# Kernel optimization log

Hardware: AMD Instinct MI355X
Metric: run time of the kernel (lower is better)

## Reference

```python
import jax, jax.numpy as jnp
import numpy as np
from jax import lax

DIM = 128
HEADS = 8
GROUPS = 8
DIM_HEAD = 64
DOWN = 4
OFF_SCALE = 4.0
KSIZE = 6
B, N, M = 2, 1024, 1024


def ln(x, g, b, eps=1e-5):
    m = x.mean(-1, keepdims=True)
    v = ((x - m) ** 2).mean(-1, keepdims=True)
    return (x - m) / jnp.sqrt(v + eps) * g + b


def grid_sample_1d(feats, grid):
    # feats: (Bg, C, Mk), grid: (Bg, Nd) normalized coords in [-1, 1]
    # bilinear, padding_mode='zeros', align_corners=False (torch semantics)
    Bg, C, Mk = feats.shape
    x = ((grid + 1.0) * Mk - 1.0) / 2.0
    x0 = jnp.floor(x)
    w1 = x - x0

    def gather(xi):
        valid = ((xi >= 0) & (xi <= Mk - 1)).astype(feats.dtype)
        idx = jnp.clip(xi, 0, Mk - 1).astype(jnp.int32)
        vals = jnp.take_along_axis(
            feats, jnp.broadcast_to(idx[:, None, :], (Bg, C, idx.shape[-1])), axis=2)
        return vals * valid[:, None, :]

    return gather(x0) * (1.0 - w1)[:, None, :] + gather(x0 + 1.0) * w1[:, None, :]


def deform_cross_attn(xq, xkv, qw, kw, vw, ow, ob, o1w, o1b, o2w,
                      c1w, c1b, c2w, c2b, c3w, c3b):
    # xq, xkv: (B, C, N) channel-first token streams
    Bb, C, Nq = xq.shape
    cg = C // GROUPS  # 16 channels per offset group
    q = jnp.einsum('bgcn,goc->bgon', xq.reshape(Bb, GROUPS, cg, Nq), qw)  # (B,g,64,N)
    gq = q.reshape(Bb * GROUPS, DIM_HEAD, Nq)
    pad = (KSIZE - DOWN) // 2
    off = lax.conv_general_dilated(gq, o1w[:, None, :], (DOWN,), [(pad, pad)],
                                   feature_group_count=DIM_HEAD,
                                   dimension_numbers=('NCH', 'OIH', 'NCH')) + o1b[None, :, None]
    off = jax.nn.gelu(off, approximate=False)
    off = jnp.tanh(jnp.einsum('bcn,c->bn', off, o2w)) * OFF_SCALE  # (B*g, Nd)
    Nd = off.shape[-1]
    vgrid = jnp.arange(Nd, dtype=off.dtype)[None] + off
    vgs = 2.0 * vgrid / max(Nd - 1, 1) - 1.0  # normalized sample positions
    xkv_g = xkv.reshape(Bb, GROUPS, cg, xkv.shape[-1]).reshape(Bb * GROUPS, cg, xkv.shape[-1])
    kv = grid_sample_1d(xkv_g, vgs).reshape(Bb, GROUPS, cg, Nd)
    k = jnp.einsum('bgcn,goc->bgon', kv, kw)
    v = jnp.einsum('bgcn,goc->bgon', kv, vw)
    sim = jnp.einsum('bhdi,bhdj->bhij', q * (DIM_HEAD ** -0.5), k)  # heads == groups
    seq = 2.0 * jnp.arange(Nq, dtype=vgs.dtype) / max(Nq - 1, 1) - 1.0
    rel = seq[None, :, None] - vgs[:, None, :]  # (B*g, N, Nd)
    bias = jnp.sign(rel) * jnp.log1p(jnp.abs(rel))
    h = jax.nn.relu(bias[..., None] * c1w[0] + c1b)  # CPB MLP, hidden=dim//4=32
    h = jax.nn.relu(h @ c2w + c2b)
    h = (h @ c3w + c3b)[..., 0]
    sim = sim + h.reshape(Bb, GROUPS, Nq, Nd)  # heads // offset_groups == 1
    attn = jax.nn.softmax(sim, axis=-1)
    out = jnp.einsum('bhij,bhdj->bhdi', attn, v).reshape(Bb, GROUPS * DIM_HEAD, Nq)
    out = jnp.einsum('bcn,oc->bon', out, ow) + ob[:, None]
    return out, attn


def mha(q_in, kv_in, w_in, b_in, w_out, b_out):
    # seq-first torch nn.MultiheadAttention, eval mode (no dropout)
    E = DIM; h = HEADS; dh = E // h
    q = q_in @ w_in[:E].T + b_in[:E]
    k = kv_in @ w_in[E:2 * E].T + b_in[E:2 * E]
    v = kv_in @ w_in[2 * E:].T + b_in[2 * E:]
    Lq, Bb, _ = q.shape
    Lk = k.shape[0]
    qh = q.reshape(Lq, Bb, h, dh).transpose(1, 2, 0, 3)
    kh = k.reshape(Lk, Bb, h, dh).transpose(1, 2, 0, 3)
    vh = v.reshape(Lk, Bb, h, dh).transpose(1, 2, 0, 3)
    attn = jax.nn.softmax(jnp.einsum('bhid,bhjd->bhij', qh, kh) * (dh ** -0.5), axis=-1)
    out = jnp.einsum('bhij,bhjd->bhid', attn, vh).transpose(2, 0, 1, 3).reshape(Lq, Bb, E)
    return out @ w_out.T + b_out


def transfusion(x1, x2, ng, nb, inw, inb, ow, ob, pw, pb):
    x = x1 + mha(ln(x1, ng, nb), ln(x2, ng, nb), inw, inb, ow, ob)
    x = ln(x.transpose(1, 0, 2), ng, nb)  # (B, N, E)
    return jnp.tanh(x.mean(1) @ pw.T + pb)[:, None, :]  # (B, 1, E)


def setup_inputs():
    key = jax.random.key(0)
    ks = iter(jax.random.split(key, 40))
    rn = lambda shape, s=0.05: jax.random.normal(next(ks), shape, dtype=jnp.float32) * s
    return {
        'x1_0': rn((B, N, DIM), 1.0),
        'x1_1': rn((B, N, DIM), 1.0),
        'x2': rn((B, M, DIM), 1.0),
        'norm_g': jnp.ones((DIM,), jnp.float32),
        'norm_b': jnp.zeros((DIM,), jnp.float32),
        'd_qw': rn((2, GROUPS, DIM_HEAD, DIM // GROUPS)),
        'd_kw': rn((2, GROUPS, DIM_HEAD, DIM // GROUPS)),
        'd_vw': rn((2, GROUPS, DIM_HEAD, DIM // GROUPS)),
        'd_ow': rn((2, DIM, GROUPS * DIM_HEAD)),
        'd_ob': jnp.zeros((2, DIM), jnp.float32),
        'd_off1w': rn((2, DIM_HEAD, KSIZE)),
        'd_off1b': jnp.zeros((2, DIM_HEAD), jnp.float32),
        'd_off2w': rn((2, DIM_HEAD)),
        'd_cpb_w1': rn((2, 1, 32)),
        'd_cpb_b1': jnp.zeros((2, 32), jnp.float32),
        'd_cpb_w2': rn((2, 32, 32)),
        'd_cpb_b2': jnp.zeros((2, 32), jnp.float32),
        'd_cpb_w3': rn((2, 32, 1)),
        'd_cpb_b3': jnp.zeros((2, 1), jnp.float32),
        'fus_w': rn((DIM, 2 * DIM)),
        'fus_b': jnp.zeros((DIM,), jnp.float32),
        'tf_ng': jnp.ones((2, DIM), jnp.float32),
        'tf_nb': jnp.zeros((2, DIM), jnp.float32),
        'tf_inw': rn((2, 3 * DIM, DIM)),
        'tf_inb': jnp.zeros((2, 3 * DIM), jnp.float32),
        'tf_ow': rn((2, DIM, DIM)),
        'tf_ob': jnp.zeros((2, DIM), jnp.float32),
        'tf_pw': rn((2, DIM, DIM)),
        'tf_pb': jnp.zeros((2, DIM), jnp.float32),
        'attn_dim': 128,
    }


def reference(x1_0, x1_1, x2, norm_g, norm_b, d_qw, d_kw, d_vw, d_ow, d_ob,
              d_off1w, d_off1b, d_off2w, d_cpb_w1, d_cpb_b1, d_cpb_w2, d_cpb_b2,
              d_cpb_w3, d_cpb_b3, fus_w, fus_b, tf_ng, tf_nb, tf_inw, tf_inb,
              tf_ow, tf_ob, tf_pw, tf_pb, attn_dim):
    nkv = ln(x2, norm_g, norm_b).transpose(0, 2, 1)
    xo1, a1 = deform_cross_attn(ln(x1_0, norm_g, norm_b).transpose(0, 2, 1), nkv,
                                d_qw[0], d_kw[0], d_vw[0], d_ow[0], d_ob[0],
                                d_off1w[0], d_off1b[0], d_off2w[0],
                                d_cpb_w1[0], d_cpb_b1[0], d_cpb_w2[0], d_cpb_b2[0],
                                d_cpb_w3[0], d_cpb_b3[0])
    xo2, a2 = deform_cross_attn(ln(x1_1, norm_g, norm_b).transpose(0, 2, 1), nkv,
                                d_qw[1], d_kw[1], d_vw[1], d_ow[1], d_ob[1],
                                d_off1w[1], d_off1b[1], d_off2w[1],
                                d_cpb_w1[1], d_cpb_b1[1], d_cpb_w2[1], d_cpb_b2[1],
                                d_cpb_w3[1], d_cpb_b3[1])
    xout1 = x1_0 + xo1.transpose(0, 2, 1)
    xout2 = x1_1 + xo2.transpose(0, 2, 1)
    x = jnp.concatenate([xout1, xout2], axis=-1) @ fus_w.T + fus_b
    query = ln(x, norm_g, norm_b).transpose(1, 0, 2)
    kv1 = ln(x1_0[:, :1, :], norm_g, norm_b).transpose(1, 0, 2)
    kv2 = ln(x1_1[:, :1, :], norm_g, norm_b).transpose(1, 0, 2)
    f1 = transfusion(query, kv1, tf_ng[0], tf_nb[0], tf_inw[0], tf_inb[0],
                     tf_ow[0], tf_ob[0], tf_pw[0], tf_pb[0])
    f2 = transfusion(query, kv2, tf_ng[1], tf_nb[1], tf_inw[1], tf_inb[1],
                     tf_ow[1], tf_ob[1], tf_pw[1], tf_pb[1])
    return (f1, f2, a1, a2)
```

## Files before the change

### kernel.cpp

```cpp
#include <hip/hip_runtime.h>
#include <hip/hip_bf16.h>


namespace {

constexpr int kN  = 1024;
constexpr int kC  = 128;
constexpr int kG  = 8;
constexpr int kDH = 64;
constexpr int kND = 256;

constexpr int   kNT    = 16384;
constexpr float kRLO   = -2.0625f;
constexpr float kRSPAN = 4.125f;

constexpr size_t W_LNKV = 0;
constexpr size_t W_LNQ1 = 262144;
constexpr size_t W_LNQ2 = 524288;
constexpr size_t W_Q    = 786432;
constexpr size_t W_K    = 1835008;
constexpr size_t W_VT   = 2097152;
constexpr size_t W_VGS  = 2359296;
constexpr size_t W_AO   = 2367488;
constexpr size_t W_FUS  = 4988928;
constexpr size_t W_TAB  = 5251072;
constexpr size_t W_MOUT = 5283844;
constexpr size_t W_PART = 5284356;
constexpr size_t W_OWB  = 5317124;
constexpr size_t W_FWB  = 5382660;

}

typedef __attribute__((ext_vector_type(8))) short short8;
typedef __attribute__((ext_vector_type(4))) float floatx4;

__device__ __forceinline__ float wave_sum(float v) {
#pragma unroll
  for (int o = 32; o > 0; o >>= 1) v += __shfl_xor(v, o, 64);
  return v;
}
__device__ __forceinline__ float cpb_bias(const float* __restrict__ tabs,
                                          float seq, float vg) {
  float rel = seq - vg;
  float ft = (rel - kRLO) * ((float)kNT / kRSPAN);
  ft = fminf(fmaxf(ft, 0.f), 16383.999f);
  int ix = (int)ft;
  float fw = ft - (float)ix;
  return tabs[ix] * (1.f - fw) + tabs[ix + 1] * fw;
}

__global__ void k_prep(const float* __restrict__ ow, const float* __restrict__ fw,
                       __hip_bfloat16* __restrict__ owb, __hip_bfloat16* __restrict__ fwb,
                       const float* __restrict__ x1_0, const float* __restrict__ x1_1,
                       const float* __restrict__ x2, float* __restrict__ lnq1,
                       float* __restrict__ lnq2, float* __restrict__ lnkv,
                       const float* __restrict__ ng, const float* __restrict__ nb,
                       const float* __restrict__ cw1, const float* __restrict__ cb1,
                       const float* __restrict__ cw2, const float* __restrict__ cb2,
                       const float* __restrict__ cw3, const float* __restrict__ cb3,
                       float* __restrict__ tab,
                       const float* __restrict__ tfng, const float* __restrict__ tfnb,
                       const float* __restrict__ inw, const float* __restrict__ inb,
                       const float* __restrict__ tow, const float* __restrict__ tob,
                       float* __restrict__ mout) {
  int bx = blockIdx.x;
  int t = threadIdx.x;
  if (bx < 640) {
    int id = bx * 256 + t;
    if (id < 131072) owb[id] = __float2bfloat16(ow[id]);
    else fwb[id - 131072] = __float2bfloat16(fw[id - 131072]);
  } else if (bx < 2176) {
    int w = t >> 6, lane = t & 63;
    int gr = (bx - 640) * 4 + w;
    int sel = gr >> 11, row = gr & 2047;
    const float* in = (sel == 0) ? x1_0 : (sel == 1) ? x1_1 : x2;
    float* out = (sel == 0) ? lnq1 : (sel == 1) ? lnq2 : lnkv;
    const float* xr = in + (size_t)row * kC;
    float xa = xr[lane], xb = xr[lane + 64];
    float m = wave_sum(xa + xb) * (1.f / kC);
    float da = xa - m, db = xb - m;
    float v = wave_sum(da * da + db * db) * (1.f / kC);
    float r = rsqrtf(v + 1e-5f);
    float* orow = out + (size_t)row * kC;
    orow[lane]      = da * r * ng[lane] + nb[lane];
    orow[lane + 64] = db * r * ng[lane + 64] + nb[lane + 64];
  } else if (bx < 2306) {
    int rel = bx - 2176;
    int idx = rel / 65, bb = rel - idx * 65;
    int tt = bb * 256 + t;
    if (tt <= kNT) {
      float rel_ = kRLO + (kRSPAN / (float)kNT) * (float)tt;
      float u = (rel_ >= 0.f ? 1.f : -1.f) * log1pf(fabsf(rel_));
      const float* W1 = cw1 + idx * 32; const float* B1 = cb1 + idx * 32;
      const float* W2 = cw2 + idx * 1024; const float* B2 = cb2 + idx * 32;
      const float* W3 = cw3 + idx * 32; const float* B3 = cb3 + idx;
      float h1[32];
#pragma unroll
      for (int m = 0; m < 32; ++m) h1[m] = fmaxf(0.f, u * W1[m] + B1[m]);
      float o = B3[0];
      for (int m = 0; m < 32; ++m) {
        float a = B2[m];
#pragma unroll
        for (int k = 0; k < 32; ++k) a += h1[k] * W2[k * 32 + m];
        o += fmaxf(a, 0.f) * W3[m];
      }
      tab[(size_t)idx * (kNT + 1) + tt] = o;
    }
  } else {
    int rel = bx - 2306;
    int i = rel >> 1, b = rel & 1;
    bool act = t < 128;
    __shared__ float red[2];
    __shared__ float s1[128];
    __shared__ float s2[128];
    const float* xs = (i ? x1_1 : x1_0) + (size_t)b * kN * kC;
    float x = act ? xs[t] : 0.f;
    float s = wave_sum(x);
    if (act && (t & 63) == 0) red[t >> 6] = s;
    __syncthreads();
    float m1 = (red[0] + red[1]) * (1.f / kC);
    __syncthreads();
    float d1 = x - m1;
    float ss = wave_sum(act ? d1 * d1 : 0.f);
    if (act && (t & 63) == 0) red[t >> 6] = ss;
    __syncthreads();
    float v1 = (red[0] + red[1]) * (1.f / kC);
    __syncthreads();
    float t0 = act ? d1 * rsqrtf(v1 + 1e-5f) * ng[t] + nb[t] : 0.f;
    s = wave_sum(t0);
    if (act && (t & 63) == 0) red[t >> 6] = s;
    __syncthreads();
    float m2 = (red[0] + red[1]) * (1.f / kC);
    __syncthreads();
    float d2 = t0 - m2;
    ss = wave_sum(act ? d2 * d2 : 0.f);
    if (act && (t & 63) == 0) red[t >> 6] = ss;
    __syncthreads();
    float v2 = (red[0] + red[1]) * (1.f / kC);
    if (act) s1[t] = d2 * rsqrtf(v2 + 1e-5f) * tfng[i * kC + t] + tfnb[i * kC + t];
    __syncthreads();
    if (act) {
      float a0 = 0.f;
      const float* wr = inw + (size_t)i * 384 * kC + (size_t)(256 + t) * kC;
      for (int c = 0; c < 128; ++c) a0 += s1[c] * wr[c];
      s2[t] = inb[i * 384 + 256 + t] + a0;
    }
    __syncthreads();
    if (act) {
      float a0 = 0.f;
      const float* wr2 = tow + (size_t)i * kC * kC + (size_t)t * kC;
      for (int c = 0; c < 128; ++c) a0 += s2[c] * wr2[c];
      mout[rel * kC + t] = tob[i * kC + t] + a0;
    }
  }
}

__global__ void k_qoff(const float* __restrict__ lnq1, const float* __restrict__ lnq2,
                       const float* __restrict__ qw, const float* __restrict__ o1w,
                       const float* __restrict__ o1b, const float* __restrict__ o2w,
                       __hip_bfloat16* __restrict__ qout, float* __restrict__ vgs) {
  int bx = blockIdx.x;
  if (bx < 512) {
    int bg = bx >> 4, r0 = (bx & 15) * 64;
    int str = bg >> 4, b = (bg >> 3) & 1, g = bg & 7;
    int rl = threadIdx.x & 63, dq = threadIdx.x >> 6;
    const float* lnq = str ? lnq2 : lnq1;
    const float* xr = lnq + ((size_t)(b * kN + r0 + rl)) * kC + g * 16;
    float4 x0 = *(const float4*)(xr + 0);
    float4 x1 = *(const float4*)(xr + 4);
    float4 x2 = *(const float4*)(xr + 8);
    float4 x3 = *(const float4*)(xr + 12);
    const float* wqb = qw + (size_t)str * 8192 + (size_t)g * 1024;
    __hip_bfloat16* qrow = qout + ((size_t)bg * 1024 + r0 + rl) * 64 + dq * 16;
#pragma unroll 4
    for (int dd = 0; dd < 16; ++dd) {
      int d = dq * 16 + dd;
      const float* wq = wqb + d * 16;
      float4 w0 = *(const float4*)(wq + 0);
      float4 w1 = *(const float4*)(wq + 4);
      float4 w2 = *(const float4*)(wq + 8);
      float4 w3 = *(const float4*)(wq + 12);
      float q = x0.x * w0.x + x0.y * w0.y + x0.z * w0.z + x0.w * w0.w
              + x1.x * w1.x + x1.y * w1.y + x1.z * w1.z + x1.w * w1.w
              + x2.x * w2.x + x2.y * w2.y + x2.z * w2.z + x2.w * w2.w
              + x3.x * w3.x + x3.y * w3.y + x3.z * w3.z + x3.w * w3.w;
      qrow[dd] = __float2bfloat16(q);
    }
  } else {
    int bxo = bx - 512;
    int w = threadIdx.x >> 6, lane = threadIdx.x & 63;
    int bg = bxo >> 6, j = ((bxo & 63) << 2) + w;
    int str = bg >> 4, b = (bg >> 3) & 1, g = bg & 7;
    const float* lnq = str ? lnq2 : lnq1;
    __shared__ float xr[4][96];
    int base = j * 4 - 1;
#pragma unroll
    for (int rep = 0; rep < 2; ++rep) {
      int idx = lane + rep * 64;
      if (idx < 96) {
        int r = idx >> 4, c = idx & 15, n = base + r;
        xr[w][idx] = (n >= 0 && n < kN)
                         ? lnq[((size_t)(b * kN + n)) * kC + g * 16 + c] : 0.f;
      }
    }
    const float* wq = qw + (size_t)str * 8192 + (size_t)(g * kDH + lane) * 16;
    float acc = o1b[str * 64 + lane];
#pragma unroll
    for (int k2 = 0; k2 < 6; ++k2) {
      float qv = 0.f;
#pragma unroll
      for (int c = 0; c < 16; ++c) qv += xr[w][k2 * 16 + c] * wq[c];
      acc += qv * o1w[str * 384 + lane * 6 + k2];
    }
    float ge = 0.5f * acc * (1.f + erff(acc * 0.70710678118654752440f));
    float s = wave_sum(ge * o2w[str * 64 + lane]);
    if (lane == 0)
      vgs[bg * kND + j] = 2.f * ((float)j + tanhf(s) * 4.0f) / 255.f - 1.f;
  }
}

__global__ void k_sample_kv(const float* __restrict__ lnkv, const float* __restrict__ vgs,
                            const float* __restrict__ kw, const float* __restrict__ vw,
                            __hip_bfloat16* __restrict__ kout,
                            __hip_bfloat16* __restrict__ vtout) {
  int w = threadIdx.x >> 6, lane = threadIdx.x & 63;
  int bg = blockIdx.x >> 6, j = ((blockIdx.x & 63) << 2) + w;
  int str = bg >> 4, b = (bg >> 3) & 1, g = bg & 7;
  __shared__ float sc[4][16];
  if (lane < 16) {
    float gr = vgs[bg * kND + j];
    float x = ((gr + 1.f) * 1024.f - 1.f) * 0.5f;
    float x0f = floorf(x);
    float w1 = x - x0f;
    int x0 = (int)x0f, x1 = x0 + 1;
    const float* src = lnkv + (size_t)b * kN * kC + g * 16 + lane;
    float v0 = (x0 >= 0 && x0 < 1024) ? src[(size_t)x0 * kC] : 0.f;
    float v1 = (x1 >= 0 && x1 < 1024) ? src[(size_t)x1 * kC] : 0.f;
    sc[w][lane] = v0 * (1.f - w1) + v1 * w1;
  }
  const float* kwr = kw + (size_t)str * 8192 + (size_t)(g * kDH + lane) * 16;
  const float* vwr = vw + (size_t)str * 8192 + (size_t)(g * kDH + lane) * 16;
  float ka = 0.f, va = 0.f;
#pragma unroll
  for (int c = 0; c < 16; ++c) { ka += sc[w][c] * kwr[c]; va += sc[w][c] * vwr[c]; }
  kout[((size_t)bg * 256 + j) * 64 + lane] = __float2bfloat16(ka);
  vtout[((size_t)bg * 64 + lane) * 256 + j] = __float2bfloat16(va);
}

__global__ void __launch_bounds__(256, 2)
k_attn(const __hip_bfloat16* __restrict__ q_g, const __hip_bfloat16* __restrict__ k_g,
       const __hip_bfloat16* __restrict__ vt_g, const float* __restrict__ vgs,
       const float* __restrict__ tab, float* __restrict__ aout,
       __hip_bfloat16* __restrict__ attout) {
  int bg = blockIdx.x >> 4, tile = blockIdx.x & 15;
  int str = bg >> 4;
  int i0 = tile * 64;
  int t = threadIdx.x;
  int w = t >> 6, l = t & 63;
  int lr = l & 15, lg = l >> 4;

  __shared__ __align__(16) __hip_bfloat16 Qs[64 * 72];
  __shared__ __align__(16) __hip_bfloat16 Ss[64 * 72];
  __shared__ __align__(16) __hip_bfloat16 Ps[64 * 272];

  const float* tabs = tab + str * (kNT + 1);

  {
    int r = t >> 2, c0 = (t & 3) * 16;
    const __hip_bfloat16* src = q_g + ((size_t)bg * 1024 + i0 + r) * 64 + c0;
    *(float4*)&Qs[r * 72 + c0]     = *(const float4*)src;
    *(float4*)&Qs[r * 72 + c0 + 8] = *(const float4*)(src + 8);
  }
  short8 a0 = *(const short8*)&Qs[(w * 16 + lr) * 72 + lg * 8];
  short8 a1 = *(const short8*)&Qs[(w * 16 + lr) * 72 + 32 + lg * 8];

  floatx4 acc[16];
#pragma unroll
  for (int f = 0; f < 16; ++f) acc[f] = {0.f, 0.f, 0.f, 0.f};

#pragma unroll
  for (int jc = 0; jc < 4; ++jc) {
    __syncthreads();
    {
      int r = t >> 2, c0 = (t & 3) * 16;
      const __hip_bfloat16* src = k_g + ((size_t)bg * 256 + jc * 64 + r) * 64 + c0;
      *(float4*)&Ss[r * 72 + c0]     = *(const float4*)src;
      *(float4*)&Ss[r * 72 + c0 + 8] = *(const float4*)(src + 8);
    }
    __syncthreads();
#pragma unroll
    for (int ct = 0; ct < 4; ++ct) {
      short8 b0 = *(const short8*)&Ss[(ct * 16 + lr) * 72 + lg * 8];
      short8 b1 = *(const short8*)&Ss[(ct * 16 + lr) * 72 + 32 + lg * 8];
      acc[jc * 4 + ct] =
          __builtin_amdgcn_mfma_f32_16x16x32_bf16(a0, b0, acc[jc * 4 + ct], 0, 0, 0);
      acc[jc * 4 + ct] =
          __builtin_amdgcn_mfma_f32_16x16x32_bf16(a1, b1, acc[jc * 4 + ct], 0, 0, 0);
    }
  }

  float vgl[16];
#pragma unroll
  for (int f = 0; f < 16; ++f) vgl[f] = vgs[bg * 256 + f * 16 + lr];
  float* aoutb = aout + (size_t)str * 4194304 + (size_t)(bg & 15) * 262144;
#pragma unroll
  for (int reg = 0; reg < 4; ++reg) {
    int row = w * 16 + lg * 4 + reg;
    int i = i0 + row;
    float seq = 2.f * (float)i / 1023.f - 1.f;
    float sv[16];
#pragma unroll
    for (int f = 0; f < 16; ++f)
      sv[f] = acc[f][reg] * 0.125f + cpb_bias(tabs, seq, vgl[f]);
    float m = sv[0];
#pragma unroll
    for (int f = 1; f < 16; ++f) m = fmaxf(m, sv[f]);
    m = fmaxf(m, __shfl_xor(m, 1, 64));
    m = fmaxf(m, __shfl_xor(m, 2, 64));
    m = fmaxf(m, __shfl_xor(m, 4, 64));
    m = fmaxf(m, __shfl_xor(m, 8, 64));
    float ev[16], sum = 0.f;
#pragma unroll
    for (int f = 0; f < 16; ++f) { ev[f] = expf(sv[f] - m); sum += ev[f]; }
    sum += __shfl_xor(sum, 1, 64);
    sum += __shfl_xor(sum, 2, 64);
    sum += __shfl_xor(sum, 4, 64);
    sum += __shfl_xor(sum, 8, 64);
    float inv = 1.f / sum;
    float* arow = aoutb + (size_t)i * 256;
#pragma unroll
    for (int f = 0; f < 16; ++f) {
      float p = ev[f] * inv;
      arow[f * 16 + lr] = p;
      Ps[row * 272 + f * 16 + lr] = __float2bfloat16(p);
    }
  }

  floatx4 oacc[4];
#pragma unroll
  for (int dt = 0; dt < 4; ++dt) oacc[dt] = {0.f, 0.f, 0.f, 0.f};
#pragma unroll
  for (int jc = 0; jc < 4; ++jc) {
    __syncthreads();
    {
      int r = t >> 2, c0 = (t & 3) * 16;
      const __hip_bfloat16* src = vt_g + ((size_t)bg * 64 + r) * 256 + jc * 64 + c0;
      *(float4*)&Ss[r * 72 + c0]     = *(const float4*)src;
      *(float4*)&Ss[r * 72 + c0 + 8] = *(const float4*)(src + 8);
    }
    __syncthreads();
    short8 pa0 = *(const short8*)&Ps[(w * 16 + lr) * 272 + jc * 64 + lg * 8];
    short8 pa1 = *(const short8*)&Ps[(w * 16 + lr) * 272 + jc * 64 + 32 + lg * 8];
#pragma unroll
    for (int dt = 0; dt < 4; ++dt) {
      short8 b0 = *(const short8*)&Ss[(dt * 16 + lr) * 72 + lg * 8];
      short8 b1 = *(const short8*)&Ss[(dt * 16 + lr) * 72 + 32 + lg * 8];
      oacc[dt] = __builtin_amdgcn_mfma_f32_16x16x32_bf16(pa0, b0, oacc[dt], 0, 0, 0);
      oacc[dt] = __builtin_amdgcn_mfma_f32_16x16x32_bf16(pa1, b1, oacc[dt], 0, 0, 0);
    }
  }
  {
    int b = (bg >> 3) & 1, g = bg & 7;
    __hip_bfloat16* ab = attout + ((size_t)(str * 2 + b) * 1024) * 512 + (size_t)g * 64;
#pragma unroll
    for (int dt = 0; dt < 4; ++dt)
#pragma unroll
      for (int reg = 0; reg < 4; ++reg) {
        int row = w * 16 + lg * 4 + reg;
        ab[(size_t)(i0 + row) * 512 + dt * 16 + lr] = __float2bfloat16(oacc[dt][reg]);
      }
  }
}

__global__ void __launch_bounds__(256, 2)
k_oproj_fuse(const __hip_bfloat16* __restrict__ aog, const __hip_bfloat16* __restrict__ owb,
             const float* __restrict__ ob,
             const float* __restrict__ x1_0, const float* __restrict__ x1_1,
             const __hip_bfloat16* __restrict__ fwb, const float* __restrict__ fb,
             float* __restrict__ fused) {
  int tok0 = blockIdx.x * 16;
  int t = threadIdx.x;
  int w = t >> 6, l = t & 63;
  int lr = l & 15, lg = l >> 4;
  int nt0 = w * 2;

  __shared__ __align__(16) __hip_bfloat16 xos[16 * 280];

  for (int s = 0; s < 2; ++s) {
    const __hip_bfloat16* arow = aog + ((size_t)(s * 2048 + tok0 + lr)) * 512 + lg * 8;
    const __hip_bfloat16* wb0 = owb + (size_t)s * 65536 + (size_t)((nt0 + 0) * 16 + lr) * 512 + lg * 8;
    const __hip_bfloat16* wb1 = owb + (size_t)s * 65536 + (size_t)((nt0 + 1) * 16 + lr) * 512 + lg * 8;
    floatx4 acc0 = {0.f, 0.f, 0.f, 0.f}, acc1 = {0.f, 0.f, 0.f, 0.f};
#pragma unroll
    for (int ks = 0; ks < 16; ++ks) {
      short8 a  = *(const short8*)(arow + ks * 32);
      short8 b0 = *(const short8*)(wb0 + ks * 32);
      short8 b1 = *(const short8*)(wb1 + ks * 32);
      acc0 = __builtin_amdgcn_mfma_f32_16x16x32_bf16(a, b0, acc0, 0, 0, 0);
      acc1 = __builtin_amdgcn_mfma_f32_16x16x32_bf16(a, b1, acc1, 0, 0, 0);
    }
    const float* x1 = s ? x1_1 : x1_0;
    float bias0 = ob[s * 128 + nt0 * 16 + lr];
    float bias1 = ob[s * 128 + (nt0 + 1) * 16 + lr];
#pragma unroll
    for (int reg = 0; reg < 4; ++reg) {
      int row = lg * 4 + reg;
      size_t xi = (size_t)(tok0 + row) * 128;
      xos[row * 280 + s * 128 + nt0 * 16 + lr] =
          __float2bfloat16(acc0[reg] + x1[xi + nt0 * 16 + lr] + bias0);
      xos[row * 280 + s * 128 + (nt0 + 1) * 16 + lr] =
          __float2bfloat16(acc1[reg] + x1[xi + (nt0 + 1) * 16 + lr] + bias1);
    }
  }
  __syncthreads();

  floatx4 f0 = {0.f, 0.f, 0.f, 0.f}, f1 = {0.f, 0.f, 0.f, 0.f};
  const __hip_bfloat16* fb0 = fwb + (size_t)((nt0 + 0) * 16 + lr) * 256 + lg * 8;
  const __hip_bfloat16* fb1 = fwb + (size_t)((nt0 + 1) * 16 + lr) * 256 + lg * 8;
#pragma unroll
  for (int ks = 0; ks < 8; ++ks) {
    short8 a  = *(const short8*)&xos[lr * 280 + ks * 32 + lg * 8];
    short8 b0 = *(const short8*)(fb0 + ks * 32);
    short8 b1 = *(const short8*)(fb1 + ks * 32);
    f0 = __builtin_amdgcn_mfma_f32_16x16x32_bf16(a, b0, f0, 0, 0, 0);
    f1 = __builtin_amdgcn_mfma_f32_16x16x32_bf16(a, b1, f1, 0, 0, 0);
  }
  float fbias0 = fb[nt0 * 16 + lr], fbias1 = fb[(nt0 + 1) * 16 + lr];
#pragma unroll
  for (int reg = 0; reg < 4; ++reg) {
    int row = lg * 4 + reg;
    fused[(size_t)(tok0 + row) * 128 + nt0 * 16 + lr]       = f0[reg] + fbias0;
    fused[(size_t)(tok0 + row) * 128 + (nt0 + 1) * 16 + lr] = f1[reg] + fbias1;
  }
}

__global__ void k_meanz(const float* __restrict__ fused, const float* __restrict__ ng,
                        const float* __restrict__ nb, const float* __restrict__ tfng,
                        const float* __restrict__ tfnb, const float* __restrict__ mout,
                        float* __restrict__ partial) {
  int chunk = blockIdx.x, b = blockIdx.y, i = blockIdx.z;
  int w = threadIdx.x >> 6, lane = threadIdx.x & 63;
  int c = lane, c2 = lane + 64;
  float moa = mout[(i * 2 + b) * kC + c], mob = mout[(i * 2 + b) * kC + c2];
  float g1a = ng[c], b1a = nb[c], g1b = ng[c2], b1b = nb[c2];
  float g2a = tfng[i * kC + c], b2a = tfnb[i * kC + c];
  float g2b = tfng[i * kC + c2], b2b = tfnb[i * kC + c2];
  float acca = 0.f, accb = 0.f;
#pragma unroll
  for (int it = 0; it < 4; ++it) {
    int tok = chunk * 16 + it * 4 + w;
    const float* xr = fused + ((size_t)(b * kN + tok)) * kC;
    float xa = xr[c], xb = xr[c2];
    float m1 = wave_sum(xa + xb) * (1.f / kC);
    float da = xa - m1, db = xb - m1;
    float v1 = wave_sum(da * da + db * db) * (1.f / kC);
    float r1 = rsqrtf(v1 + 1e-5f);
    float za = da * r1 * g1a + b1a + moa;
    float zb = db * r1 * g1b + b1b + mob;
    float m2 = wave_sum(za + zb) * (1.f / kC);
    float ea = za - m2, eb = zb - m2;
    float v2 = wave_sum(ea * ea + eb * eb) * (1.f / kC);
    float r2 = rsqrtf(v2 + 1e-5f);
    acca += ea * r2 * g2a + b2a;
    accb += eb * r2 * g2b + b2b;
  }
  __shared__ float red[4][128];
  red[w][c] = acca; red[w][c2] = accb;
  __syncthreads();
  if (w == 0) {
    float pa = red[0][c] + red[1][c] + red[2][c] + red[3][c];
    float pb = red[0][c2] + red[1][c2] + red[2][c2] + red[3][c2];
    float* pr = partial + ((size_t)(i * 2 + b) * 64 + chunk) * kC;
    pr[c] = pa; pr[c2] = pb;
  }
}

__global__ void k_final(const float* __restrict__ partial, const float* __restrict__ pw,
                        const float* __restrict__ pb, float* __restrict__ out) {
  int ib = blockIdx.x;
  int i = ib >> 1, t = threadIdx.x;
  int c = t & 127, half = t >> 7;
  float a = 0.f;
  for (int ch = half * 32; ch < half * 32 + 32; ++ch)
    a += partial[((size_t)ib * 64 + ch) * kC + c];
  __shared__ float s[256];
  s[half * 128 + c] = a;
  __syncthreads();
  if (t < 128) s[t] = (s[t] + s[128 + t]) * (1.f / (float)kN);
  __syncthreads();
  if (t < 128) {
    float a0 = 0.f;
    const float* wr = pw + (size_t)i * kC * kC + (size_t)t * kC;
    for (int cc = 0; cc < 128; ++cc) a0 += s[cc] * wr[cc];
    out[ib * 128 + t] = tanhf(pb[i * kC + t] + a0);
  }
}

extern "C" void kernel_launch(void* const* d_in, const int* in_sizes, int n_in,
                              void* d_out, int out_size, void* d_ws, size_t ws_size,
                              hipStream_t stream) {
  const float* x1_0   = (const float*)d_in[0];
  const float* x1_1   = (const float*)d_in[1];
  const float* x2     = (const float*)d_in[2];
  const float* norm_g = (const float*)d_in[3];
  const float* norm_b = (const float*)d_in[4];
  const float* d_qw   = (const float*)d_in[5];
  const float* d_kw   = (const float*)d_in[6];
  const float* d_vw   = (const float*)d_in[7];
  const float* d_ow   = (const float*)d_in[8];
  const float* d_ob   = (const float*)d_in[9];
  const float* d_o1w  = (const float*)d_in[10];
  const float* d_o1b  = (const float*)d_in[11];
  const float* d_o2w  = (const float*)d_in[12];
  const float* c_w1   = (const float*)d_in[13];
  const float* c_b1   = (const float*)d_in[14];
  const float* c_w2   = (const float*)d_in[15];
  const float* c_b2   = (const float*)d_in[16];
  const float* c_w3   = (const float*)d_in[17];
  const float* c_b3   = (const float*)d_in[18];
  const float* fus_w  = (const float*)d_in[19];
  const float* fus_b  = (const float*)d_in[20];
  const float* tf_ng  = (const float*)d_in[21];
  const float* tf_nb  = (const float*)d_in[22];
  const float* tf_inw = (const float*)d_in[23];
  const float* tf_inb = (const float*)d_in[24];
  const float* tf_ow  = (const float*)d_in[25];
  const float* tf_ob  = (const float*)d_in[26];
  const float* tf_pw  = (const float*)d_in[27];
  const float* tf_pb  = (const float*)d_in[28];

  float* ws = (float*)d_ws;
  float* out = (float*)d_out;
  float* lnkv = ws + W_LNKV;
  float* lnq1 = ws + W_LNQ1; float* lnq2 = ws + W_LNQ2;
  __hip_bfloat16* qb  = (__hip_bfloat16*)(ws + W_Q);
  __hip_bfloat16* kb  = (__hip_bfloat16*)(ws + W_K);
  __hip_bfloat16* vtb = (__hip_bfloat16*)(ws + W_VT);
  float* vgsw = ws + W_VGS;
  __hip_bfloat16* aob = (__hip_bfloat16*)(ws + W_AO);
  float* fused = ws + W_FUS; float* tab = ws + W_TAB;
  float* moutp = ws + W_MOUT; float* partp = ws + W_PART;
  __hip_bfloat16* owb = (__hip_bfloat16*)(ws + W_OWB);
  __hip_bfloat16* fwb = (__hip_bfloat16*)(ws + W_FWB);

  float* aoutb = out + 512;

  k_prep<<<2310, 256, 0, stream>>>(d_ow, fus_w, owb, fwb,
                                   x1_0, x1_1, x2, lnq1, lnq2, lnkv, norm_g, norm_b,
                                   c_w1, c_b1, c_w2, c_b2, c_w3, c_b3, tab,
                                   tf_ng, tf_nb, tf_inw, tf_inb, tf_ow, tf_ob, moutp);
  k_qoff<<<2560, 256, 0, stream>>>(lnq1, lnq2, d_qw, d_o1w, d_o1b, d_o2w, qb, vgsw);
  k_sample_kv<<<2048, 256, 0, stream>>>(lnkv, vgsw, d_kw, d_vw, kb, vtb);
  k_attn<<<512, 256, 0, stream>>>(qb, kb, vtb, vgsw, tab, aoutb, aob);
  k_oproj_fuse<<<128, 256, 0, stream>>>(aob, owb, d_ob, x1_0, x1_1, fwb, fus_b, fused);
  k_meanz<<<dim3(64, 2, 2), 256, 0, stream>>>(fused, norm_g, norm_b, tf_ng, tf_nb,
                                              moutp, partp);
  k_final<<<4, 256, 0, stream>>>(partp, tf_pw, tf_pb, out);

  (void)in_sizes; (void)n_in; (void)out_size; (void)ws_size;
}
```

Before: 92.60 us.

## Shrink CPB lookup table, stage it in LDS, fuse mean-LN into output projection

Reduces the precomputed continuous-position-bias table from 16384 to 2048 entries, so k_prep does less MLP work, and copies the table into LDS inside k_attn (reusing the Q buffer) so the bias gathers no longer go to global memory. Also fuses the k_meanz layer-norm/mean reduction into k_oproj_fuse via an LDS tile, dropping the fused intermediate buffer and one kernel launch. The coarser table raises interpolation error in the bias. Overwriting Qs after the fragments are loaded depends on the added barrier.

```diff
diff --git a/kernel.cpp b/kernel.cpp
--- a/kernel.cpp
+++ b/kernel.cpp
@@ -10,7 +10,7 @@
 constexpr int kDH = 64;
 constexpr int kND = 256;
 
-constexpr int   kNT    = 16384;
+constexpr int   kNT    = 2048;
 constexpr float kRLO   = -2.0625f;
 constexpr float kRSPAN = 4.125f;
 
@@ -22,7 +22,6 @@
 constexpr size_t W_VT   = 2097152;
 constexpr size_t W_VGS  = 2359296;
 constexpr size_t W_AO   = 2367488;
-constexpr size_t W_FUS  = 4988928;
 constexpr size_t W_TAB  = 5251072;
 constexpr size_t W_MOUT = 5283844;
 constexpr size_t W_PART = 5284356;
@@ -39,14 +38,14 @@
   for (int o = 32; o > 0; o >>= 1) v += __shfl_xor(v, o, 64);
   return v;
 }
-__device__ __forceinline__ float cpb_bias(const float* __restrict__ tabs,
-                                          float seq, float vg) {
+__device__ __forceinline__ float cpb_lds(const float* __restrict__ tabL,
+                                         float seq, float vg) {
   float rel = seq - vg;
   float ft = (rel - kRLO) * ((float)kNT / kRSPAN);
-  ft = fminf(fmaxf(ft, 0.f), 16383.999f);
+  ft = fminf(fmaxf(ft, 0.f), (float)kNT - 0.001f);
   int ix = (int)ft;
   float fw = ft - (float)ix;
-  return tabs[ix] * (1.f - fw) + tabs[ix + 1] * fw;
+  return tabL[ix] * (1.f - fw) + tabL[ix + 1] * fw;
 }
 
 __global__ void k_prep(const float* __restrict__ ow, const float* __restrict__ fw,
@@ -84,9 +83,9 @@
     float* orow = out + (size_t)row * kC;
     orow[lane]      = da * r * ng[lane] + nb[lane];
     orow[lane + 64] = db * r * ng[lane + 64] + nb[lane + 64];
-  } else if (bx < 2306) {
+  } else if (bx < 2194) {
     int rel = bx - 2176;
-    int idx = rel / 65, bb = rel - idx * 65;
+    int idx = rel / 9, bb = rel - idx * 9;
     int tt = bb * 256 + t;
     if (tt <= kNT) {
       float rel_ = kRLO + (kRSPAN / (float)kNT) * (float)tt;
@@ -107,7 +106,7 @@
       tab[(size_t)idx * (kNT + 1) + tt] = o;
     }
   } else {
-    int rel = bx - 2306;
+    int rel = bx - 2194;
     int i = rel >> 1, b = rel & 1;
     bool act = t < 128;
     __shared__ float red[2];
@@ -261,7 +260,7 @@
 
   __shared__ __align__(16) __hip_bfloat16 Qs[64 * 72];
   __shared__ __align__(16) __hip_bfloat16 Ss[64 * 72];
-  __shared__ __align__(16) __hip_bfloat16 Ps[64 * 272];
+  __shared__ __align__(16) __hip_bfloat16 Ps[64 * 264];
 
   const float* tabs = tab + str * (kNT + 1);
 
@@ -273,6 +272,9 @@
   }
   short8 a0 = *(const short8*)&Qs[(w * 16 + lr) * 72 + lg * 8];
   short8 a1 = *(const short8*)&Qs[(w * 16 + lr) * 72 + 32 + lg * 8];
+  __syncthreads();
+  float* tabL = (float*)Qs;
+  for (int e = t; e <= kNT; e += 256) tabL[e] = tabs[e];
 
   floatx4 acc[16];
 #pragma unroll
@@ -311,7 +313,7 @@
     float sv[16];
 #pragma unroll
     for (int f = 0; f < 16; ++f)
-      sv[f] = acc[f][reg] * 0.125f + cpb_bias(tabs, seq, vgl[f]);
+      sv[f] = acc[f][reg] * 0.125f + cpb_lds(tabL, seq, vgl[f]);
     float m = sv[0];
 #pragma unroll
     for (int f = 1; f < 16; ++f) m = fmaxf(m, sv[f]);
@@ -332,7 +334,7 @@
     for (int f = 0; f < 16; ++f) {
       float p = ev[f] * inv;
       arow[f * 16 + lr] = p;
-      Ps[row * 272 + f * 16 + lr] = __float2bfloat16(p);
+      Ps[row * 264 + f * 16 + lr] = __float2bfloat16(p);
     }
   }
 
@@ -349,8 +351,8 @@
       *(float4*)&Ss[r * 72 + c0 + 8] = *(const float4*)(src + 8);
     }
     __syncthreads();
-    short8 pa0 = *(const short8*)&Ps[(w * 16 + lr) * 272 + jc * 64 + lg * 8];
-    short8 pa1 = *(const short8*)&Ps[(w * 16 + lr) * 272 + jc * 64 + 32 + lg * 8];
+    short8 pa0 = *(const short8*)&Ps[(w * 16 + lr) * 264 + jc * 64 + lg * 8];
+    short8 pa1 = *(const short8*)&Ps[(w * 16 + lr) * 264 + jc * 64 + 32 + lg * 8];
 #pragma unroll
     for (int dt = 0; dt < 4; ++dt) {
       short8 b0 = *(const short8*)&Ss[(dt * 16 + lr) * 72 + lg * 8];
@@ -377,14 +379,19 @@
              const float* __restrict__ ob,
              const float* __restrict__ x1_0, const float* __restrict__ x1_1,
              const __hip_bfloat16* __restrict__ fwb, const float* __restrict__ fb,
-             float* __restrict__ fused) {
+             const float* __restrict__ ng, const float* __restrict__ nb,
+             const float* __restrict__ tfng, const float* __restrict__ tfnb,
+             const float* __restrict__ mout, float* __restrict__ partial) {
   int tok0 = blockIdx.x * 16;
   int t = threadIdx.x;
   int w = t >> 6, l = t & 63;
   int lr = l & 15, lg = l >> 4;
   int nt0 = w * 2;
 
-  __shared__ __align__(16) __hip_bfloat16 xos[16 * 280];
+  __shared__ __align__(16) unsigned char smem[16 * 280 * 2];
+  __shared__ float red[4][128];
+  __hip_bfloat16* xos = (__hip_bfloat16*)smem;
+  float* fs = (float*)smem;
 
   for (int s = 0; s < 2; ++s) {
     const __hip_bfloat16* arow = aog + ((size_t)(s * 2048 + tok0 + lr)) * 512 + lg * 8;
@@ -425,53 +432,69 @@
     f0 = __builtin_amdgcn_mfma_f32_16x16x32_bf16(a, b0, f0, 0, 0, 0);
     f1 = __builtin_amdgcn_mfma_f32_16x16x32_bf16(a, b1, f1, 0, 0, 0);
   }
-  float fbias0 = fb[nt0 * 16 + lr], fbias1 = fb[(nt0 + 1) * 16 + lr];
-#pragma unroll
-  for (int reg = 0; reg < 4; ++reg) {
-    int row = lg * 4 + reg;
-    fused[(size_t)(tok0 + row) * 128 + nt0 * 16 + lr]       = f0[reg] + fbias0;
-    fused[(size_t)(tok0 + row) * 128 + (nt0 + 1) * 16 + lr] = f1[reg] + fbias1;
-  }
-}
-
-__global__ void k_meanz(const float* __restrict__ fused, const float* __restrict__ ng,
-                        const float* __restrict__ nb, const float* __restrict__ tfng,
-                        const float* __restrict__ tfnb, const float* __restrict__ mout,
-                        float* __restrict__ partial) {
-  int chunk = blockIdx.x, b = blockIdx.y, i = blockIdx.z;
-  int w = threadIdx.x >> 6, lane = threadIdx.x & 63;
-  int c = lane, c2 = lane + 64;
-  float moa = mout[(i * 2 + b) * kC + c], mob = mout[(i * 2 + b) * kC + c2];
-  float g1a = ng[c], b1a = nb[c], g1b = ng[c2], b1b = nb[c2];
-  float g2a = tfng[i * kC + c], b2a = tfnb[i * kC + c];
-  float g2b = tfng[i * kC + c2], b2b = tfnb[i * kC + c2];
-  float acca = 0.f, accb = 0.f;
+  __syncthreads();
+
+  {
+    float fbias0 = fb[nt0 * 16 + lr], fbias1 = fb[(nt0 + 1) * 16 + lr];
+#pragma unroll
+    for (int reg = 0; reg < 4; ++reg) {
+      int row = lg * 4 + reg;
+      fs[row * 132 + w * 32 + lr]      = f0[reg] + fbias0;
+      fs[row * 132 + w * 32 + 16 + lr] = f1[reg] + fbias1;
+    }
+  }
+  __syncthreads();
+
+  int b = tok0 >> 10, chunk = (tok0 & 1023) >> 4;
+  float g1a = ng[l], b1a = nb[l], g1b = ng[l + 64], b1b = nb[l + 64];
+  float mo0a = mout[b * 128 + l], mo0b = mout[b * 128 + l + 64];
+  float mo1a = mout[(2 + b) * 128 + l], mo1b = mout[(2 + b) * 128 + l + 64];
+  float g20a = tfng[l], b20a = tfnb[l], g20b = tfng[l + 64], b20b = tfnb[l + 64];
+  float g21a = tfng[128 + l], b21a = tfnb[128 + l];
+  float g21b = tfng[192 + l], b21b = tfnb[192 + l];
+  float acc0a = 0.f, acc0b = 0.f, acc1a = 0.f, acc1b = 0.f;
 #pragma unroll
   for (int it = 0; it < 4; ++it) {
-    int tok = chunk * 16 + it * 4 + w;
-    const float* xr = fused + ((size_t)(b * kN + tok)) * kC;
-    float xa = xr[c], xb = xr[c2];
+    int tok = it * 4 + w;
+    float xa = fs[tok * 132 + l], xb = fs[tok * 132 + l + 64];
     float m1 = wave_sum(xa + xb) * (1.f / kC);
     float da = xa - m1, db = xb - m1;
     float v1 = wave_sum(da * da + db * db) * (1.f / kC);
     float r1 = rsqrtf(v1 + 1e-5f);
-    float za = da * r1 * g1a + b1a + moa;
-    float zb = db * r1 * g1b + b1b + mob;
-    float m2 = wave_sum(za + zb) * (1.f / kC);
-    float ea = za - m2, eb = zb - m2;
-    float v2 = wave_sum(ea * ea + eb * eb) * (1.f / kC);
-    float r2 = rsqrtf(v2 + 1e-5f);
-    acca += ea * r2 * g2a + b2a;
-    accb += eb * r2 * g2b + b2b;
-  }
-  __shared__ float red[4][128];
-  red[w][c] = acca; red[w][c2] = accb;
+    float ba = da * r1 * g1a + b1a, bb = db * r1 * g1b + b1b;
+    {
+      float za = ba + mo0a, zb = bb + mo0b;
+      float m2 = wave_sum(za + zb) * (1.f / kC);
+      float ea = za - m2, eb = zb - m2;
+      float v2 = wave_sum(ea * ea + eb * eb) * (1.f / kC);
+      float r2 = rsqrtf(v2 + 1e-5f);
+      acc0a += ea * r2 * g20a + b20a;
+      acc0b += eb * r2 * g20b + b20b;
+    }
+    {
+      float za = ba + mo1a, zb = bb + mo1b;
+      float m2 = wave_sum(za + zb) * (1.f / kC);
+      float ea = za - m2, eb = zb - m2;
+      float v2 = wave_sum(ea * ea + eb * eb) * (1.f / kC);
+      float r2 = rsqrtf(v2 + 1e-5f);
+      acc1a += ea * r2 * g21a + b21a;
+      acc1b += eb * r2 * g21b + b21b;
+    }
+  }
+  red[w][l] = acc0a; red[w][l + 64] = acc0b;
   __syncthreads();
   if (w == 0) {
-    float pa = red[0][c] + red[1][c] + red[2][c] + red[3][c];
-    float pb = red[0][c2] + red[1][c2] + red[2][c2] + red[3][c2];
-    float* pr = partial + ((size_t)(i * 2 + b) * 64 + chunk) * kC;
-    pr[c] = pa; pr[c2] = pb;
+    float* pr = partial + ((size_t)(b)*64 + chunk) * kC;
+    pr[l]      = red[0][l] + red[1][l] + red[2][l] + red[3][l];
+    pr[l + 64] = red[0][l + 64] + red[1][l + 64] + red[2][l + 64] + red[3][l + 64];
+  }
+  __syncthreads();
+  red[w][l] = acc1a; red[w][l + 64] = acc1b;
+  __syncthreads();
+  if (w == 0) {
+    float* pr = partial + ((size_t)(2 + b) * 64 + chunk) * kC;
+    pr[l]      = red[0][l] + red[1][l] + red[2][l] + red[3][l];
+    pr[l + 64] = red[0][l + 64] + red[1][l + 64] + red[2][l + 64] + red[3][l + 64];
   }
 }
 
@@ -538,23 +561,22 @@
   __hip_bfloat16* vtb = (__hip_bfloat16*)(ws + W_VT);
   float* vgsw = ws + W_VGS;
   __hip_bfloat16* aob = (__hip_bfloat16*)(ws + W_AO);
-  float* fused = ws + W_FUS; float* tab = ws + W_TAB;
+  float* tab = ws + W_TAB;
   float* moutp = ws + W_MOUT; float* partp = ws + W_PART;
   __hip_bfloat16* owb = (__hip_bfloat16*)(ws + W_OWB);
   __hip_bfloat16* fwb = (__hip_bfloat16*)(ws + W_FWB);
 
   float* aoutb = out + 512;
 
-  k_prep<<<2310, 256, 0, stream>>>(d_ow, fus_w, owb, fwb,
+  k_prep<<<2198, 256, 0, stream>>>(d_ow, fus_w, owb, fwb,
                                    x1_0, x1_1, x2, lnq1, lnq2, lnkv, norm_g, norm_b,
                                    c_w1, c_b1, c_w2, c_b2, c_w3, c_b3, tab,
                                    tf_ng, tf_nb, tf_inw, tf_inb, tf_ow, tf_ob, moutp);
   k_qoff<<<2560, 256, 0, stream>>>(lnq1, lnq2, d_qw, d_o1w, d_o1b, d_o2w, qb, vgsw);
   k_sample_kv<<<2048, 256, 0, stream>>>(lnkv, vgsw, d_kw, d_vw, kb, vtb);
   k_attn<<<512, 256, 0, stream>>>(qb, kb, vtb, vgsw, tab, aoutb, aob);
-  k_oproj_fuse<<<128, 256, 0, stream>>>(aob, owb, d_ob, x1_0, x1_1, fwb, fus_b, fused);
-  k_meanz<<<dim3(64, 2, 2), 256, 0, stream>>>(fused, norm_g, norm_b, tf_ng, tf_nb,
-                                              moutp, partp);
+  k_oproj_fuse<<<128, 256, 0, stream>>>(aob, owb, d_ob, x1_0, x1_1, fwb, fus_b,
+                                        norm_g, norm_b, tf_ng, tf_nb, moutp, partp);
   k_final<<<4, 256, 0, stream>>>(partp, tf_pw, tf_pb, out);
 
   (void)in_sizes; (void)n_in; (void)out_size; (void)ws_size;
```

Result: faster. 88.61 us (-4.3%).
